# Performance work log

Hardware: AMD Instinct MI355X
Metric: run time of the kernel (lower is better)

## Reference

```python
import jax, jax.numpy as jnp
import numpy as np

N, E, IN, HID, H, C, L, G = 20000, 640000, 128, 256, 8, 32, 5, 64
NEG_SLOPE = 0.2


def _layernorm(x, g, b, eps=1e-5):
    mu = jnp.mean(x, axis=-1, keepdims=True)
    var = jnp.mean((x - mu) ** 2, axis=-1, keepdims=True)
    return (x - mu) * jax.lax.rsqrt(var + eps) * g + b


def _gatv2(h, src, dst, Wl, bl, Wr, br, att, out_bias):
    # h: [N, HID]; src/dst: [E+N] (self loops appended)
    n = h.shape[0]
    xl = (h @ Wl + bl).reshape(n, H, C)  # source transform
    xr = (h @ Wr + br).reshape(n, H, C)  # target transform
    e = jax.nn.leaky_relu(xl[src] + xr[dst], NEG_SLOPE)       # [Etot, H, C]
    logits = jnp.einsum('ehc,hc->eh', e, att)                  # [Etot, H]
    m = jax.ops.segment_max(logits, dst, num_segments=n)       # segment softmax over dst
    a = jnp.exp(logits - m[dst])
    s = jax.ops.segment_sum(a, dst, num_segments=n)
    alpha = a / (s[dst] + 1e-16)                               # [Etot, H]
    out = jax.ops.segment_sum(alpha[:, :, None] * xl[src], dst, num_segments=n)
    return out.reshape(n, HID) + out_bias


def setup_inputs() -> dict:
    key = jax.random.key(0)
    ks = jax.random.split(key, 16)
    sc = 0.05
    inp = {
        'x': jax.random.normal(ks[0], (N, IN), jnp.float32),
        'edge_index': jax.random.randint(ks[1], (2, E), 0, N, jnp.int64),
        'batch': jnp.sort(jax.random.randint(ks[2], (N,), 0, G, jnp.int64)),
        'proj_W': jax.random.normal(ks[3], (IN, HID), jnp.float32) * sc,
        'proj_b': jnp.zeros((HID,), jnp.float32),
        'Wl': jax.random.normal(ks[4], (L, HID, HID), jnp.float32) * sc,
        'bl': jnp.zeros((L, HID), jnp.float32),
        'Wr': jax.random.normal(ks[5], (L, HID, HID), jnp.float32) * sc,
        'br': jnp.zeros((L, HID), jnp.float32),
        'att': jax.random.normal(ks[6], (L, H, C), jnp.float32) * sc,
        'out_bias': jnp.zeros((L, HID), jnp.float32),
        'ln_g': jnp.ones((L, HID), jnp.float32),
        'ln_b': jnp.zeros((L, HID), jnp.float32),
    }
    return inp


def reference(x, edge_index, batch, proj_W, proj_b, Wl, bl, Wr, br, att, out_bias, ln_g, ln_b):
    n = x.shape[0]
    loops = jnp.arange(n, dtype=edge_index.dtype)
    src = jnp.concatenate([edge_index[0], loops])  # add_self_loops=True
    dst = jnp.concatenate([edge_index[1], loops])
    h = x @ proj_W + proj_b
    for i in range(L):  # dropout = identity in eval mode
        conv = _gatv2(h, src, dst, Wl[i], bl[i], Wr[i], br[i], att[i], out_bias[i])
        h = _layernorm(h + jax.nn.elu(conv), ln_g[i], ln_b[i])
    counts = jax.ops.segment_sum(jnp.ones((n,), h.dtype), batch, num_segments=G)
    gsum = jax.ops.segment_sum(h, batch, num_segments=G)
    graph_emb = gsum / jnp.maximum(counts, 1.0)[:, None]  # global_mean_pool
    return graph_emb, h, batch
```

## Files before the change

### kernel.cpp

```cpp
#include <hip/hip_runtime.h>
#include <hip/hip_bf16.h>

#define NN   20000
#define NE   640000
#define INF_ 128
#define HID  256
#define NL   5
#define NG   64

typedef __hip_bfloat16 bf16;
typedef __attribute__((ext_vector_type(4))) float f32x4;
typedef __attribute__((ext_vector_type(8))) short bf16x8;

#if __has_builtin(__builtin_amdgcn_exp2f)
#define EXP2F __builtin_amdgcn_exp2f
#else
#define EXP2F exp2f
#endif

__device__ __forceinline__ float b2f(bf16 v) { return __bfloat162float(v); }
__device__ __forceinline__ short f2bs(float v) {
  union { bf16 h; short s; } u; u.h = __float2bfloat16(v); return u.s;
}
__device__ __forceinline__ f32x4 ldbf4o(const char* __restrict__ basep, unsigned off) {
  const uint2 u = *(const uint2*)(basep + off);
  f32x4 r;
  r[0] = __uint_as_float(u.x << 16);
  r[1] = __uint_as_float(u.x & 0xffff0000u);
  r[2] = __uint_as_float(u.y << 16);
  r[3] = __uint_as_float(u.y & 0xffff0000u);
  return r;
}

#if __has_builtin(__builtin_amdgcn_update_dpp)
template<int CTRL>
__device__ __forceinline__ float dpp_add(float v) {
  int t = __builtin_amdgcn_update_dpp(0, __float_as_int(v), CTRL, 0xF, 0xF, true);
  return v + __int_as_float(t);
}
__device__ __forceinline__ float hsum8(float v) {
  v = dpp_add<0xB1>(v);
  v = dpp_add<0x4E>(v);
  v = dpp_add<0x141>(v);
  return v;
}
__device__ __forceinline__ float wsum64(float v) {
  v = hsum8(v);
  v = dpp_add<0x140>(v);
  v += __shfl_xor(v, 16);
  v += __shfl_xor(v, 32);
  return v;
}
#else
__device__ __forceinline__ float hsum8(float v) {
  v += __shfl_xor(v, 1);  v += __shfl_xor(v, 2);  v += __shfl_xor(v, 4);
  return v;
}
__device__ __forceinline__ float wsum64(float v) {
  v += __shfl_xor(v, 1);  v += __shfl_xor(v, 2);  v += __shfl_xor(v, 4);
  v += __shfl_xor(v, 8);  v += __shfl_xor(v, 16); v += __shfl_xor(v, 32);
  return v;
}
#endif

__global__ void detect_kernel(const int* __restrict__ ei,
                              const int* __restrict__ batch,
                              int* __restrict__ flags) {
  if (blockIdx.x == 0) {
    const int k = threadIdx.x;
    const bool e_bad = (k < 40) && (ei[2 * (k * 15999) + 1] != 0);
    const bool b_bad = (k < 40) && (batch[2 * (k * 249) + 1] != 0);
    const int e64 = __any(e_bad) ? 0 : 1;
    const int b64 = __any(b_bad) ? 0 : 1;
    if (k == 0) { flags[0] = e64; flags[1] = b64; }
  }
}

__device__ __forceinline__ int ld_i(const int* p, int f, size_t idx) {
  return f ? p[2 * idx] : p[idx];
}

__global__ void hist_kernel(const int* __restrict__ ei, const int* __restrict__ flags,
                            int* __restrict__ deg) {
  int e = blockIdx.x * blockDim.x + threadIdx.x;
  if (e >= NE) return;
  int f = flags[0];
  int d = ld_i(ei, f, (size_t)NE + e);
  if ((unsigned)d < NN) atomicAdd(&deg[d], 1);
}

#define SCAN_NB ((NN + 255) / 256)
__global__ __launch_bounds__(256) void scan1_kernel(
    const int* __restrict__ deg, int* __restrict__ off, int* __restrict__ bsum)
{
  __shared__ int sh[256];
  const int t = threadIdx.x;
  const int i = blockIdx.x * 256 + t;
  const int v = (i < NN) ? deg[i] : 0;
  sh[t] = v;
  __syncthreads();
  for (int d = 1; d < 256; d <<= 1) {
    int nv = (t >= d) ? sh[t - d] : 0;
    __syncthreads();
    sh[t] += nv;
    __syncthreads();
  }
  if (i < NN) off[i] = sh[t] - v;
  if (t == 255) bsum[blockIdx.x] = sh[255];
}

__global__ __launch_bounds__(128) void scan2_kernel(
    const int* __restrict__ bsum, int* __restrict__ boff, int* __restrict__ off)
{
  __shared__ int sh[128];
  const int t = threadIdx.x;
  const int v = (t < SCAN_NB) ? bsum[t] : 0;
  sh[t] = v;
  __syncthreads();
  for (int d = 1; d < 128; d <<= 1) {
    int nv = (t >= d) ? sh[t - d] : 0;
    __syncthreads();
    sh[t] += nv;
    __syncthreads();
  }
  if (t < SCAN_NB) boff[t] = sh[t] - v;
  if (t == SCAN_NB - 1) off[NN] = sh[t];
}

__global__ __launch_bounds__(256) void scan3_kernel(
    int* __restrict__ off, const int* __restrict__ boff, int* __restrict__ tmp)
{
  const int i = blockIdx.x * 256 + threadIdx.x;
  if (i < NN) {
    const int val = off[i] + boff[blockIdx.x];
    off[i] = val;
    tmp[i] = val;
  }
}

__global__ void scatter_kernel(const int* __restrict__ ei, const int* __restrict__ flags,
                               int* __restrict__ tmp, int* __restrict__ csr) {
  int e = blockIdx.x * blockDim.x + threadIdx.x;
  if (e >= NE) return;
  int f = flags[0];
  int d = ld_i(ei, f, (size_t)NE + e);
  int s = ld_i(ei, f, (size_t)e);
  if ((unsigned)d < NN) {
    int p = atomicAdd(&tmp[d], 1);
    int sv = ((unsigned)s < NN) ? s : 0;
    if ((unsigned)p < NE) csr[p] = sv * (HID * 2);
  }
}

__global__ __launch_bounds__(256) void xbf_kernel(
    const float* __restrict__ x, short* __restrict__ x_bf)
{
  const int i = blockIdx.x * 256 + threadIdx.x;
  if (i >= NN * INF_ / 8) return;
  const float* s = x + (size_t)i * 8;
  f32x4 lo = *(const f32x4*)s;
  f32x4 hi = *(const f32x4*)(s + 4);
  bf16x8 v;
#pragma unroll
  for (int j = 0; j < 4; ++j) { v[j] = f2bs(lo[j]); v[4 + j] = f2bs(hi[j]); }
  *(bf16x8*)&x_bf[(size_t)i * 8] = v;
}

__global__ __launch_bounds__(256) void prep_btf_kernel(
    const float* __restrict__ Wl, const float* __restrict__ Wr,
    const float* __restrict__ projW,
    short* __restrict__ BTl, short* __restrict__ BTr, short* __restrict__ BTp)
{
  const int z = blockIdx.y;
  const int g = blockIdx.x * 256 + threadIdx.x;
  if (z == 2 * NL) {
    if (g >= 4096) return;
    const int ln   = g & 63;
    const int frag = (g >> 6) & 31;
    const int half = g >> 11;
    const int nf = frag >> 2, kk = frag & 3;
    const int n  = half * 128 + nf * 16 + (ln & 15);
    const int k0 = kk * 32 + (ln >> 4) * 8;
    bf16x8 outv;
#pragma unroll
    for (int j = 0; j < 8; ++j) outv[j] = f2bs(projW[(size_t)(k0 + j) * HID + n]);
    *(bf16x8*)&BTp[(size_t)g * 8] = outv;
    return;
  }
  const float* src = (z < NL) ? Wl + (size_t)z * HID * HID
                              : Wr + (size_t)(z - NL) * HID * HID;
  short* dst = (z < NL) ? BTl + (size_t)z * HID * HID
                        : BTr + (size_t)(z - NL) * HID * HID;
  const int ln   = g & 63;
  const int frag = (g >> 6) & 63;
  const int half = g >> 12;
  const int nf = frag >> 3, kk = frag & 7;
  const int n  = half * 128 + nf * 16 + (ln & 15);
  const int k0 = kk * 32 + (ln >> 4) * 8;
  bf16x8 outv;
#pragma unroll
  for (int j = 0; j < 8; ++j) outv[j] = f2bs(src[(size_t)(k0 + j) * HID + n]);
  *(bf16x8*)&dst[(size_t)g * 8] = outv;
}

template<int K, bool A_BF16>
__global__ __launch_bounds__(256) void gemm_bias_kernel(
    const void* __restrict__ Av, const float* __restrict__ B,
    const float* __restrict__ bias, float* __restrict__ Cf,
    bf16* __restrict__ Cb, int M)
{
  constexpr int N = 256;
  constexpr int LDB = K + 8;
  __shared__ __align__(16) short bT[32 * LDB];
  const int tid = threadIdx.x;
  const int n0 = blockIdx.x * 32;
  const int m_base = blockIdx.y * 256;

  if (tid < K) {
    const float* brow = B + (size_t)tid * N + n0;
#pragma unroll
    for (int j = 0; j < 32; ++j) bT[j * LDB + tid] = f2bs(brow[j]);
  }
  __syncthreads();

  const int wave = tid >> 6;
  const int lane = tid & 63;
  const int r    = lane & 15;
  const int quad = lane >> 4;
  const int m_wave = m_base + wave * 64;

  f32x4 acc[4][2];
#pragma unroll
  for (int i = 0; i < 4; ++i) { acc[i][0] = (f32x4)0.0f; acc[i][1] = (f32x4)0.0f; }

#pragma unroll
  for (int kk = 0; kk < K / 32; ++kk) {
    const int kof = kk * 32 + quad * 8;
    bf16x8 b0 = *(const bf16x8*)&bT[r * LDB + kof];
    bf16x8 b1 = *(const bf16x8*)&bT[(r + 16) * LDB + kof];
#pragma unroll
    for (int sm = 0; sm < 4; ++sm) {
      const int row = m_wave + sm * 16 + r;
      bf16x8 a = (bf16x8)(short)0;
      if (row < M) {
        if constexpr (A_BF16) {
          a = *(const bf16x8*)((const short*)Av + (size_t)row * K + kof);
        } else {
          const float* ap = (const float*)Av + (size_t)row * K + kof;
          f32x4 lo = *(const f32x4*)ap;
          f32x4 hi = *(const f32x4*)(ap + 4);
#pragma unroll
          for (int j = 0; j < 4; ++j) { a[j] = f2bs(lo[j]); a[4 + j] = f2bs(hi[j]); }
        }
      }
      acc[sm][0] = __builtin_amdgcn_mfma_f32_16x16x32_bf16(a, b0, acc[sm][0], 0, 0, 0);
      acc[sm][1] = __builtin_amdgcn_mfma_f32_16x16x32_bf16(a, b1, acc[sm][1], 0, 0, 0);
    }
  }

  const float bv0 = bias[n0 + r];
  const float bv1 = bias[n0 + 16 + r];
#pragma unroll
  for (int sm = 0; sm < 4; ++sm) {
#pragma unroll
    for (int rg = 0; rg < 4; ++rg) {
      const int row = m_wave + sm * 16 + quad * 4 + rg;
      if (row < M) {
        size_t i0 = (size_t)row * N + n0 + r;
        float v0 = acc[sm][0][rg] + bv0;
        float v1 = acc[sm][1][rg] + bv1;
        if (Cf) { Cf[i0] = v0; Cf[i0 + 16] = v1; }
        if (Cb) {
          ((unsigned short*)Cb)[i0]      = (unsigned short)f2bs(v0);
          ((unsigned short*)Cb)[i0 + 16] = (unsigned short)f2bs(v1);
        }
      }
    }
  }
}

template<bool A_BF16>
__global__ __launch_bounds__(256) void gemm_dual_kernel(
    const void* __restrict__ Av,
    const float* __restrict__ Bl, const float* __restrict__ Br,
    const float* __restrict__ bl, const float* __restrict__ br,
    bf16* __restrict__ Cl, bf16* __restrict__ Cr, int M)
{
  constexpr int K = HID, N = 256;
  constexpr int LDB = K + 8;
  __shared__ __align__(16) short bTl[32 * LDB];
  __shared__ __align__(16) short bTr[32 * LDB];
  const int tid = threadIdx.x;
  const int n0 = blockIdx.x * 32;
  const int m_base = blockIdx.y * 256;

  {
    const float* browl = Bl + (size_t)tid * N + n0;
    const float* browr = Br + (size_t)tid * N + n0;
#pragma unroll
    for (int j = 0; j < 32; ++j) {
      bTl[j * LDB + tid] = f2bs(browl[j]);
      bTr[j * LDB + tid] = f2bs(browr[j]);
    }
  }
  __syncthreads();

  const int wave = tid >> 6;
  const int lane = tid & 63;
  const int r    = lane & 15;
  const int quad = lane >> 4;
  const int m_wave = m_base + wave * 64;

  f32x4 accl[4][2], accr[4][2];
#pragma unroll
  for (int i = 0; i < 4; ++i) {
    accl[i][0] = (f32x4)0.0f; accl[i][1] = (f32x4)0.0f;
    accr[i][0] = (f32x4)0.0f; accr[i][1] = (f32x4)0.0f;
  }

#pragma unroll
  for (int kk = 0; kk < K / 32; ++kk) {
    const int kof = kk * 32 + quad * 8;
    bf16x8 b0l = *(const bf16x8*)&bTl[r * LDB + kof];
    bf16x8 b1l = *(const bf16x8*)&bTl[(r + 16) * LDB + kof];
    bf16x8 b0r = *(const bf16x8*)&bTr[r * LDB + kof];
    bf16x8 b1r = *(const bf16x8*)&bTr[(r + 16) * LDB + kof];
#pragma unroll
    for (int sm = 0; sm < 4; ++sm) {
      const int row = m_wave + sm * 16 + r;
      bf16x8 a = (bf16x8)(short)0;
      if (row < M) {
        if constexpr (A_BF16) {
          a = *(const bf16x8*)((const short*)Av + (size_t)row * K + kof);
        } else {
          const float* ap = (const float*)Av + (size_t)row * K + kof;
          f32x4 lo = *(const f32x4*)ap;
          f32x4 hi = *(const f32x4*)(ap + 4);
#pragma unroll
          for (int j = 0; j < 4; ++j) { a[j] = f2bs(lo[j]); a[4 + j] = f2bs(hi[j]); }
        }
      }
      accl[sm][0] = __builtin_amdgcn_mfma_f32_16x16x32_bf16(a, b0l, accl[sm][0], 0, 0, 0);
      accl[sm][1] = __builtin_amdgcn_mfma_f32_16x16x32_bf16(a, b1l, accl[sm][1], 0, 0, 0);
      accr[sm][0] = __builtin_amdgcn_mfma_f32_16x16x32_bf16(a, b0r, accr[sm][0], 0, 0, 0);
      accr[sm][1] = __builtin_amdgcn_mfma_f32_16x16x32_bf16(a, b1r, accr[sm][1], 0, 0, 0);
    }
  }

  const float bl0v = bl[n0 + r],  bl1v = bl[n0 + 16 + r];
  const float br0v = br[n0 + r],  br1v = br[n0 + 16 + r];
#pragma unroll
  for (int sm = 0; sm < 4; ++sm) {
#pragma unroll
    for (int rg = 0; rg < 4; ++rg) {
      const int row = m_wave + sm * 16 + quad * 4 + rg;
      if (row < M) {
        size_t i0 = (size_t)row * N + n0 + r;
        ((unsigned short*)Cl)[i0]      = (unsigned short)f2bs(accl[sm][0][rg] + bl0v);
        ((unsigned short*)Cl)[i0 + 16] = (unsigned short)f2bs(accl[sm][1][rg] + bl1v);
        ((unsigned short*)Cr)[i0]      = (unsigned short)f2bs(accr[sm][0][rg] + br0v);
        ((unsigned short*)Cr)[i0 + 16] = (unsigned short)f2bs(accr[sm][1][rg] + br1v);
      }
    }
  }
}

__global__ __launch_bounds__(256) void gemm_dual_tiled64_kernel(
    const short* __restrict__ Ab,
    const short* __restrict__ BTl, const short* __restrict__ BTr,
    const float* __restrict__ bl, const float* __restrict__ br,
    bf16* __restrict__ Cl, bf16* __restrict__ Cr, int M)
{
  constexpr int K = HID;
  __shared__ __align__(16) short bfr[16384];
  const int tid  = threadIdx.x;
  const int lane = tid & 63;
  const int wv   = tid >> 6;
  const int bx   = blockIdx.x;
  const int q    = bx & 3;
  const int n0   = q * 64;
  const short* BTf = (bx < 4) ? BTl : BTr;
  const float* bias = (bx < 4) ? bl : br;
  bf16* C = (bx < 4) ? Cl : Cr;
  const int half   = q >> 1;
  const int nfbase = (q & 1) * 4;
  const short* src = BTf + (size_t)half * 32768;

#pragma unroll
  for (int it = 0; it < 8; ++it) {
    const int c   = it * 256 + tid;
    const int f   = c >> 6;
    const int ln  = c & 63;
    const int nfL = f >> 3, kk = f & 7;
    const int gfrag = (nfbase + nfL) * 8 + kk;
    *(bf16x8*)&bfr[(size_t)c * 8] = *(const bf16x8*)&src[((size_t)gfrag * 64 + ln) * 8];
  }

  const int r    = lane & 15;
  const int quad = lane >> 4;
  const int m_wave = blockIdx.y * 128 + wv * 32;

  const int ar0 = min(m_wave + r, M - 1);
  const int ar1 = min(m_wave + 16 + r, M - 1);
  const short* a0p = Ab + (size_t)ar0 * K + quad * 8;
  const short* a1p = Ab + (size_t)ar1 * K + quad * 8;
  bf16x8 a0[8], a1[8];
#pragma unroll
  for (int kk = 0; kk < 8; ++kk) {
    a0[kk] = *(const bf16x8*)(a0p + kk * 32);
    a1[kk] = *(const bf16x8*)(a1p + kk * 32);
  }

  __syncthreads();

  f32x4 acc[2][4];
#pragma unroll
  for (int sm = 0; sm < 2; ++sm)
#pragma unroll
    for (int nf = 0; nf < 4; ++nf) acc[sm][nf] = (f32x4)0.0f;

#pragma unroll
  for (int kk = 0; kk < 8; ++kk) {
#pragma unroll
    for (int nf = 0; nf < 4; ++nf) {
      const bf16x8 b = *(const bf16x8*)&bfr[((nf * 8 + kk) * 64 + lane) * 8];
      acc[0][nf] = __builtin_amdgcn_mfma_f32_16x16x32_bf16(a0[kk], b, acc[0][nf], 0, 0, 0);
      acc[1][nf] = __builtin_amdgcn_mfma_f32_16x16x32_bf16(a1[kk], b, acc[1][nf], 0, 0, 0);
    }
  }

  float bv[4];
#pragma unroll
  for (int nf = 0; nf < 4; ++nf) bv[nf] = bias[n0 + nf * 16 + r];

#pragma unroll
  for (int sm = 0; sm < 2; ++sm) {
#pragma unroll
    for (int rg = 0; rg < 4; ++rg) {
      const int row = m_wave + sm * 16 + quad * 4 + rg;
      if (row < M) {
        unsigned short* cp = (unsigned short*)C + (size_t)row * 256 + n0 + r;
#pragma unroll
        for (int nf = 0; nf < 4; ++nf)
          cp[nf * 16] = (unsigned short)f2bs(acc[sm][nf][rg] + bv[nf]);
      }
    }
  }
}

__global__ __launch_bounds__(256) void gemm_proj_tiled_kernel(
    const short* __restrict__ Ax,
    const short* __restrict__ BTp,
    const float* __restrict__ bias, float* __restrict__ Cf,
    bf16* __restrict__ Cb, int M)
{
  constexpr int K = INF_;
  __shared__ __align__(16) short bfr[16384];
  const int tid  = threadIdx.x;
  const int lane = tid & 63;
  const int wv   = tid >> 6;
  const int bx   = blockIdx.x;
  const int n0   = bx * 128;
  const short* src = BTp + (size_t)bx * 16384;

#pragma unroll
  for (int it = 0; it < 8; ++it) {
    const int c = it * 256 + tid;
    *(bf16x8*)&bfr[(size_t)c * 8] = *(const bf16x8*)&src[(size_t)c * 8];
  }

  const int r    = lane & 15;
  const int quad = lane >> 4;
  const int m_wave = blockIdx.y * 128 + wv * 32;

  const int ar0 = min(m_wave + r, M - 1);
  const int ar1 = min(m_wave + 16 + r, M - 1);
  const short* a0p = Ax + (size_t)ar0 * K + quad * 8;
  const short* a1p = Ax + (size_t)ar1 * K + quad * 8;
  bf16x8 a0[4], a1[4];
#pragma unroll
  for (int kk = 0; kk < 4; ++kk) {
    a0[kk] = *(const bf16x8*)(a0p + kk * 32);
    a1[kk] = *(const bf16x8*)(a1p + kk * 32);
  }

  __syncthreads();

  f32x4 acc[2][8];
#pragma unroll
  for (int sm = 0; sm < 2; ++sm)
#pragma unroll
    for (int nf = 0; nf < 8; ++nf) acc[sm][nf] = (f32x4)0.0f;

#pragma unroll
  for (int kk = 0; kk < 4; ++kk) {
#pragma unroll
    for (int nf = 0; nf < 8; ++nf) {
      const bf16x8 b = *(const bf16x8*)&bfr[((nf * 4 + kk) * 64 + lane) * 8];
      acc[0][nf] = __builtin_amdgcn_mfma_f32_16x16x32_bf16(a0[kk], b, acc[0][nf], 0, 0, 0);
      acc[1][nf] = __builtin_amdgcn_mfma_f32_16x16x32_bf16(a1[kk], b, acc[1][nf], 0, 0, 0);
    }
  }

  float bv[8];
#pragma unroll
  for (int nf = 0; nf < 8; ++nf) bv[nf] = bias[n0 + nf * 16 + r];

#pragma unroll
  for (int sm = 0; sm < 2; ++sm) {
#pragma unroll
    for (int rg = 0; rg < 4; ++rg) {
      const int row = m_wave + sm * 16 + quad * 4 + rg;
      if (row < M) {
        const size_t i0 = (size_t)row * 256 + n0 + r;
#pragma unroll
        for (int nf = 0; nf < 8; ++nf) {
          const float v = acc[sm][nf][rg] + bv[nf];
          Cf[i0 + nf * 16] = v;
          ((unsigned short*)Cb)[i0 + nf * 16] = (unsigned short)f2bs(v);
        }
      }
    }
  }
}

__global__ __launch_bounds__(256) void gat_layer_kernel(
    const bf16* __restrict__ xl, const bf16* __restrict__ xr,
    float* __restrict__ h, bf16* __restrict__ h_bf,
    const int* __restrict__ off, const int* __restrict__ csr,
    const float* __restrict__ att, const float* __restrict__ outb,
    const float* __restrict__ lng, const float* __restrict__ lnb)
{
  const int lane = threadIdx.x & 63;
  const int node = __builtin_amdgcn_readfirstlane(blockIdx.x * 4 + (threadIdx.x >> 6));
  const int cb   = ((lane >> 3) << 5) + ((lane & 7) << 2);
  const unsigned cb2  = (unsigned)cb * 2;
  const unsigned selfo = (unsigned)node * (HID * 2) + cb2;
  const size_t base = (size_t)node * HID + cb;
  const char* xlc = (const char*)xl;

  const f32x4 xrv = ldbf4o((const char*)xr, selfo);
  const f32x4 xls = ldbf4o(xlc, selfo);
  const f32x4 av = *(const f32x4*)(att + cb);
  f32x4 a6, a4;
#pragma unroll
  for (int c = 0; c < 4; ++c) {
    a6[c] = av[c] * (0.6f * 1.44269504f);
    a4[c] = av[c] * (0.4f * 1.44269504f);
  }

  const f32x4 ob = *(const f32x4*)(outb + cb);
  const f32x4 hv = *(const f32x4*)(h + base);
  const f32x4 g4 = *(const f32x4*)(lng + cb);
  const f32x4 b4 = *(const f32x4*)(lnb + cb);

  float pa = 0.f;
#pragma unroll
  for (int c = 0; c < 4; ++c) {
    float z = xls[c] + xrv[c];
    pa = fmaf(a6[c], z, pa);
    pa = fmaf(a4[c], fabsf(z), pa);
  }
  const float es = EXP2F(hsum8(pa));
  float s = es;
  f32x4 o;
#pragma unroll
  for (int c = 0; c < 4; ++c) o[c] = es * xls[c];

  int beg = __builtin_amdgcn_readfirstlane(off[node]);
  int end = __builtin_amdgcn_readfirstlane(off[node + 1]);
  if (beg < 0) beg = 0;
  if (end > NE) end = NE;
  const unsigned* csrb = (const unsigned*)csr;

  const int nblk = (end > beg) ? ((end - beg) >> 3) : 0;
  unsigned nx[8];
  if (nblk > 0) {
#pragma unroll
    for (int j = 0; j < 8; ++j) nx[j] = csrb[beg + j];
  }
  for (int b = 0; b < nblk; ++b) {
    f32x4 xv[8];
#pragma unroll
    for (int j = 0; j < 8; ++j) xv[j] = ldbf4o(xlc, nx[j] + cb2);
    if (b + 1 < nblk) {
      const int pn = beg + (b + 1) * 8;
#pragma unroll
      for (int j = 0; j < 8; ++j) nx[j] = csrb[pn + j];
    }
    float e[8];
#pragma unroll
    for (int j = 0; j < 8; ++j) {
      float acc = 0.f;
#pragma unroll
      for (int c = 0; c < 4; ++c) {
        float z = xv[j][c] + xrv[c];
        acc = fmaf(a6[c], z, acc);
        acc = fmaf(a4[c], fabsf(z), acc);
      }
      e[j] = EXP2F(hsum8(acc));
    }
    s += (((e[0] + e[1]) + (e[2] + e[3])) + ((e[4] + e[5]) + (e[6] + e[7])));
#pragma unroll
    for (int c = 0; c < 4; ++c) {
      float c0 = fmaf(e[0], xv[0][c], fmaf(e[1], xv[1][c],
                 fmaf(e[2], xv[2][c], fmaf(e[3], xv[3][c], o[c]))));
      float c1 = fmaf(e[4], xv[4][c], fmaf(e[5], xv[5][c],
                 fmaf(e[6], xv[6][c], e[7] * xv[7][c])));
      o[c] = c0 + c1;
    }
  }
  for (int p = beg + nblk * 8; p < end; ++p) {
    const unsigned oo = csrb[p] + cb2;
    const f32x4 xv = ldbf4o(xlc, oo);
    float pe = 0.f;
#pragma unroll
    for (int c = 0; c < 4; ++c) {
      float z = xv[c] + xrv[c];
      pe = fmaf(a6[c], z, pe);
      pe = fmaf(a4[c], fabsf(z), pe);
    }
    const float ee = EXP2F(hsum8(pe));
    s += ee;
#pragma unroll
    for (int c = 0; c < 4; ++c) o[c] = fmaf(ee, xv[c], o[c]);
  }

  const float inv_s = 1.f / s;
  f32x4 res;
#pragma unroll
  for (int c = 0; c < 4; ++c) {
    float conv = fmaf(o[c], inv_s, ob[c]);
    float el = conv > 0.f ? conv : (__expf(conv) - 1.f);
    res[c] = hv[c] + el;
  }
  float pr = (res[0] + res[1]) + (res[2] + res[3]);
  const float mu = wsum64(pr) * (1.f / 256.f);
  f32x4 dv;
  float p2s = 0.f;
#pragma unroll
  for (int c = 0; c < 4; ++c) { dv[c] = res[c] - mu; p2s = fmaf(dv[c], dv[c], p2s); }
  const float var = wsum64(p2s) * (1.f / 256.f);
  const float rs = rsqrtf(var + 1e-5f);
  f32x4 y;
#pragma unroll
  for (int c = 0; c < 4; ++c) y[c] = fmaf(dv[c] * rs, g4[c], b4[c]);

  *(f32x4*)(h + base) = y;
  if (h_bf) {
    ushort4 u;
    u.x = (unsigned short)f2bs(y[0]);
    u.y = (unsigned short)f2bs(y[1]);
    u.z = (unsigned short)f2bs(y[2]);
    u.w = (unsigned short)f2bs(y[3]);
    *(ushort4*)((unsigned short*)h_bf + base) = u;
  }
}

__global__ __launch_bounds__(256) void pool_kernel(
    const float* __restrict__ h, const int* __restrict__ batch,
    const int* __restrict__ flags, float* __restrict__ gsum, int* __restrict__ gcnt)
{
  const int t = threadIdx.x;
  const int f = flags[1];
  int n0 = blockIdx.x * 80;
  int n1 = n0 + 80; if (n1 > NN) n1 = NN;
  float acc = 0.f;
  int g_cur = ld_i(batch, f, n0);
  if ((unsigned)g_cur >= NG) g_cur = 0;
  int run = 0;
  for (int n = n0; n < n1; ++n) {
    int g = ld_i(batch, f, n);
    if ((unsigned)g >= NG) g = 0;
    if (g != g_cur) {
      atomicAdd(&gsum[(size_t)g_cur * HID + t], acc);
      if (t == 0) atomicAdd(&gcnt[g_cur], run);
      acc = 0.f; run = 0; g_cur = g;
    }
    acc += h[(size_t)n * HID + t];
    ++run;
  }
  atomicAdd(&gsum[(size_t)g_cur * HID + t], acc);
  if (t == 0) atomicAdd(&gcnt[g_cur], run);
}

__global__ void write_out_kernel(const float* __restrict__ gsum, const int* __restrict__ gcnt,
                                 const int* __restrict__ batch,
                                 const int* __restrict__ flags, float* __restrict__ out)
{
  int i = blockIdx.x * blockDim.x + threadIdx.x;
  if (i < NG * HID) {
    int g = i >> 8;
    float c = (float)gcnt[g];
    c = c > 1.f ? c : 1.f;
    out[i] = gsum[i] / c;
  } else if (i < NG * HID + NN) {
    int n = i - NG * HID;
    int f = flags[1];
    out[(size_t)NG * HID + (size_t)NN * HID + n] = (float)ld_i(batch, f, (size_t)n);
  }
}

extern "C" void kernel_launch(void* const* d_in, const int* in_sizes, int n_in,
                              void* d_out, int out_size, void* d_ws, size_t ws_size,
                              hipStream_t stream) {
  (void)in_sizes; (void)n_in; (void)out_size;

  const float* x     = (const float*)d_in[0];
  const int*   ei    = (const int*)d_in[1];
  const int*   batch = (const int*)d_in[2];
  const float* projW = (const float*)d_in[3];
  const float* projB = (const float*)d_in[4];
  const float* Wl    = (const float*)d_in[5];
  const float* bl    = (const float*)d_in[6];
  const float* Wr    = (const float*)d_in[7];
  const float* br    = (const float*)d_in[8];
  const float* att   = (const float*)d_in[9];
  const float* outb  = (const float*)d_in[10];
  const float* lng   = (const float*)d_in[11];
  const float* lnb   = (const float*)d_in[12];
  float* out = (float*)d_out;

  float* h = out + (size_t)NG * HID;

  char* ws = (char*)d_ws;
  size_t o = 0;
  auto alloc = [&](size_t bytes) -> void* {
    void* p = ws + o;
    o += (bytes + 255) & ~(size_t)255;
    return p;
  };
  int*   flags = (int*)alloc(4 * 4);
  int*   deg   = (int*)alloc((size_t)NN * 4);
  int*   offs  = (int*)alloc((size_t)(NN + 1) * 4);
  int*   tmp   = (int*)alloc((size_t)NN * 4);
  float* gsum  = (float*)alloc((size_t)NG * HID * 4);
  int*   gcnt  = (int*)alloc((size_t)NG * 4);
  int*   bsum  = (int*)alloc((size_t)(SCAN_NB + 1) * 4);
  int*   boff  = (int*)alloc((size_t)(SCAN_NB + 1) * 4);
  int*   csr   = (int*)alloc((size_t)NE * 4);
  bf16*  xl    = (bf16*)alloc((size_t)NN * HID * 2);
  bf16*  xr    = (bf16*)alloc((size_t)NN * HID * 2);
  size_t o_base = o;
  bf16*  h_bf  = (bf16*)alloc((size_t)NN * HID * 2);
  const bool use_hbf = (ws_size >= o);
  if (!use_hbf) { h_bf = nullptr; o = o_base; }
  size_t o_hbf = o;
  short* BTl = (short*)alloc((size_t)NL * HID * HID * 2);
  short* BTr = (short*)alloc((size_t)NL * HID * HID * 2);
  const bool use_bt = use_hbf && (ws_size >= o);
  if (!use_bt) { o = o_hbf; }
  size_t o_bt = o;
  short* x_bf = (short*)alloc((size_t)NN * INF_ * 2);
  short* BTp  = (short*)alloc((size_t)HID * INF_ * 2);
  const bool use_xbf = use_bt && (ws_size >= o);
  if (!use_xbf) { o = o_bt; }

  hipMemsetAsync(deg, 0, (size_t)NN * 4, stream);
  hipMemsetAsync(gsum, 0, (size_t)NG * HID * 4 + (size_t)NG * 4, stream);

  detect_kernel<<<1, 64, 0, stream>>>(ei, batch, flags);

  if (use_bt) {
    dim3 pg(32, 2 * NL + (use_xbf ? 1 : 0));
    prep_btf_kernel<<<pg, 256, 0, stream>>>(Wl, Wr, projW, BTl, BTr, BTp);
  }
  if (use_xbf) {
    xbf_kernel<<<(NN * INF_ / 8 + 255) / 256, 256, 0, stream>>>(x, x_bf);
  }

  hist_kernel<<<(NE + 255) / 256, 256, 0, stream>>>(ei, flags, deg);
  scan1_kernel<<<SCAN_NB, 256, 0, stream>>>(deg, offs, bsum);
  scan2_kernel<<<1, 128, 0, stream>>>(bsum, boff, offs);
  scan3_kernel<<<SCAN_NB, 256, 0, stream>>>(offs, boff, tmp);
  scatter_kernel<<<(NE + 255) / 256, 256, 0, stream>>>(ei, flags, tmp, csr);

  dim3 gg(HID / 32, (NN + 255) / 256);

  if (use_xbf) {
    dim3 gp(2, (NN + 127) / 128);
    gemm_proj_tiled_kernel<<<gp, 256, 0, stream>>>(x_bf, BTp, projB, h, h_bf, NN);
  } else {
    gemm_bias_kernel<INF_, false><<<gg, 256, 0, stream>>>(x, projW, projB, h, h_bf, NN);
  }

  dim3 gt(8, (NN + 127) / 128);
  for (int i = 0; i < NL; ++i) {
    if (use_bt) {
      gemm_dual_tiled64_kernel<<<gt, 256, 0, stream>>>((const short*)h_bf,
          BTl + (size_t)i * HID * HID, BTr + (size_t)i * HID * HID,
          bl + (size_t)i * HID, br + (size_t)i * HID, xl, xr, NN);
    } else if (use_hbf) {
      gemm_dual_kernel<true><<<gg, 256, 0, stream>>>(h_bf,
          Wl + (size_t)i * HID * HID, Wr + (size_t)i * HID * HID,
          bl + (size_t)i * HID, br + (size_t)i * HID, xl, xr, NN);
    } else {
      gemm_dual_kernel<false><<<gg, 256, 0, stream>>>(h,
          Wl + (size_t)i * HID * HID, Wr + (size_t)i * HID * HID,
          bl + (size_t)i * HID, br + (size_t)i * HID, xl, xr, NN);
    }
    gat_layer_kernel<<<NN / 4, 256, 0, stream>>>(xl, xr, h, h_bf, offs, csr,
                                                 att + (size_t)i * HID, outb + (size_t)i * HID,
                                                 lng + (size_t)i * HID, lnb + (size_t)i * HID);
  }

  pool_kernel<<<250, 256, 0, stream>>>(h, batch, flags, gsum, gcnt);
  write_out_kernel<<<(NG * HID + NN + 255) / 256, 256, 0, stream>>>(gsum, gcnt, batch, flags, out);
}
```

Baseline: 522.9 us.

## Double-buffer weight tiles in dual GEMM, halve grid width, reuse A fragments

The dual GEMM kernel now has each block compute 128 output columns in two 64-column passes. The second weight tile is prefetched into registers during the first pass, then staged into a second LDS buffer. The A-row fragments loaded into registers are reused across both passes, halving redundant A loads, and the grid x dimension drops from 8 to 4. The cost is doubled LDS per block (64KB) and extra registers, which may reduce occupancy. There are also fewer blocks to fill the GPU.

```diff
diff --git a/kernel.cpp b/kernel.cpp
--- a/kernel.cpp
+++ b/kernel.cpp
@@ -365,35 +365,29 @@
   }
 }
 
-__global__ __launch_bounds__(256) void gemm_dual_tiled64_kernel(
+__global__ __launch_bounds__(256) void gemm_dual_db_kernel(
     const short* __restrict__ Ab,
     const short* __restrict__ BTl, const short* __restrict__ BTr,
     const float* __restrict__ bl, const float* __restrict__ br,
     bf16* __restrict__ Cl, bf16* __restrict__ Cr, int M)
 {
   constexpr int K = HID;
-  __shared__ __align__(16) short bfr[16384];
+  __shared__ __align__(16) short buf0[16384];
+  __shared__ __align__(16) short buf1[16384];
   const int tid  = threadIdx.x;
   const int lane = tid & 63;
   const int wv   = tid >> 6;
   const int bx   = blockIdx.x;
-  const int q    = bx & 3;
-  const int n0   = q * 64;
-  const short* BTf = (bx < 4) ? BTl : BTr;
-  const float* bias = (bx < 4) ? bl : br;
-  bf16* C = (bx < 4) ? Cl : Cr;
-  const int half   = q >> 1;
-  const int nfbase = (q & 1) * 4;
-  const short* src = BTf + (size_t)half * 32768;
+  const int half = bx & 1;
+  const short* BTf = (bx < 2) ? BTl : BTr;
+  const float* bias = (bx < 2) ? bl : br;
+  bf16* C = (bx < 2) ? Cl : Cr;
+  const short* img = BTf + (size_t)half * 32768;
 
 #pragma unroll
   for (int it = 0; it < 8; ++it) {
-    const int c   = it * 256 + tid;
-    const int f   = c >> 6;
-    const int ln  = c & 63;
-    const int nfL = f >> 3, kk = f & 7;
-    const int gfrag = (nfbase + nfL) * 8 + kk;
-    *(bf16x8*)&bfr[(size_t)c * 8] = *(const bf16x8*)&src[((size_t)gfrag * 64 + ln) * 8];
+    const int c = it * 256 + tid;
+    *(bf16x8*)&buf0[(size_t)c * 8] = *(const bf16x8*)&img[(size_t)c * 8];
   }
 
   const int r    = lane & 15;
@@ -411,6 +405,13 @@
     a1[kk] = *(const bf16x8*)(a1p + kk * 32);
   }
 
+  bf16x8 q1r[8];
+#pragma unroll
+  for (int it = 0; it < 8; ++it) {
+    const int c = it * 256 + tid;
+    q1r[it] = *(const bf16x8*)&img[(size_t)(2048 + c) * 8];
+  }
+
   __syncthreads();
 
   f32x4 acc[2][4];
@@ -423,26 +424,70 @@
   for (int kk = 0; kk < 8; ++kk) {
 #pragma unroll
     for (int nf = 0; nf < 4; ++nf) {
-      const bf16x8 b = *(const bf16x8*)&bfr[((nf * 8 + kk) * 64 + lane) * 8];
+      const bf16x8 b = *(const bf16x8*)&buf0[((nf * 8 + kk) * 64 + lane) * 8];
       acc[0][nf] = __builtin_amdgcn_mfma_f32_16x16x32_bf16(a0[kk], b, acc[0][nf], 0, 0, 0);
       acc[1][nf] = __builtin_amdgcn_mfma_f32_16x16x32_bf16(a1[kk], b, acc[1][nf], 0, 0, 0);
     }
   }
 
-  float bv[4];
-#pragma unroll
-  for (int nf = 0; nf < 4; ++nf) bv[nf] = bias[n0 + nf * 16 + r];
-
-#pragma unroll
-  for (int sm = 0; sm < 2; ++sm) {
-#pragma unroll
-    for (int rg = 0; rg < 4; ++rg) {
-      const int row = m_wave + sm * 16 + quad * 4 + rg;
-      if (row < M) {
-        unsigned short* cp = (unsigned short*)C + (size_t)row * 256 + n0 + r;
-#pragma unroll
-        for (int nf = 0; nf < 4; ++nf)
-          cp[nf * 16] = (unsigned short)f2bs(acc[sm][nf][rg] + bv[nf]);
+  {
+    const int n0 = half * 128;
+    float bv[4];
+#pragma unroll
+    for (int nf = 0; nf < 4; ++nf) bv[nf] = bias[n0 + nf * 16 + r];
+#pragma unroll
+    for (int sm = 0; sm < 2; ++sm) {
+#pragma unroll
+      for (int rg = 0; rg < 4; ++rg) {
+        const int row = m_wave + sm * 16 + quad * 4 + rg;
+        if (row < M) {
+          unsigned short* cp = (unsigned short*)C + (size_t)row * 256 + n0 + r;
+#pragma unroll
+          for (int nf = 0; nf < 4; ++nf)
+            cp[nf * 16] = (unsigned short)f2bs(acc[sm][nf][rg] + bv[nf]);
+        }
+      }
+    }
+  }
+
+#pragma unroll
+  for (int it = 0; it < 8; ++it) {
+    const int c = it * 256 + tid;
+    *(bf16x8*)&buf1[(size_t)c * 8] = q1r[it];
+  }
+  __syncthreads();
+
+#pragma unroll
+  for (int sm = 0; sm < 2; ++sm)
+#pragma unroll
+    for (int nf = 0; nf < 4; ++nf) acc[sm][nf] = (f32x4)0.0f;
+
+#pragma unroll
+  for (int kk = 0; kk < 8; ++kk) {
+#pragma unroll
+    for (int nf = 0; nf < 4; ++nf) {
+      const bf16x8 b = *(const bf16x8*)&buf1[((nf * 8 + kk) * 64 + lane) * 8];
+      acc[0][nf] = __builtin_amdgcn_mfma_f32_16x16x32_bf16(a0[kk], b, acc[0][nf], 0, 0, 0);
+      acc[1][nf] = __builtin_amdgcn_mfma_f32_16x16x32_bf16(a1[kk], b, acc[1][nf], 0, 0, 0);
+    }
+  }
+
+  {
+    const int n0 = half * 128 + 64;
+    float bv[4];
+#pragma unroll
+    for (int nf = 0; nf < 4; ++nf) bv[nf] = bias[n0 + nf * 16 + r];
+#pragma unroll
+    for (int sm = 0; sm < 2; ++sm) {
+#pragma unroll
+      for (int rg = 0; rg < 4; ++rg) {
+        const int row = m_wave + sm * 16 + quad * 4 + rg;
+        if (row < M) {
+          unsigned short* cp = (unsigned short*)C + (size_t)row * 256 + n0 + r;
+#pragma unroll
+          for (int nf = 0; nf < 4; ++nf)
+            cp[nf * 16] = (unsigned short)f2bs(acc[sm][nf][rg] + bv[nf]);
+        }
       }
     }
   }
@@ -784,10 +829,10 @@
     gemm_bias_kernel<INF_, false><<<gg, 256, 0, stream>>>(x, projW, projB, h, h_bf, NN);
   }
 
-  dim3 gt(8, (NN + 127) / 128);
+  dim3 gt(4, (NN + 127) / 128);
   for (int i = 0; i < NL; ++i) {
     if (use_bt) {
-      gemm_dual_tiled64_kernel<<<gt, 256, 0, stream>>>((const short*)h_bf,
+      gemm_dual_db_kernel<<<gt, 256, 0, stream>>>((const short*)h_bf,
           BTl + (size_t)i * HID * HID, BTr + (size_t)i * HID * HID,
           bl + (size_t)i * HID, br + (size_t)i * HID, xl, xr, NN);
     } else if (use_hbf) {
```

Measured after the change: 517.0 us. Within noise of the previous version (-1.1%).
